# Kernel optimization log

Measured on AMD Instinct MI355X. Metric: run time of the kernel, lower is better.

The kernel has to match this reference:

```python
import jax, jax.numpy as jnp
import numpy as np

B, A, IN, H, NA = 256, 32, 512, 512, 64


def setup_inputs() -> dict:
    key = jax.random.key(0)
    ks = jax.random.split(key, 9)
    s = 1.0 / np.sqrt(H).astype(np.float32)
    si = 1.0 / np.sqrt(IN).astype(np.float32)
    return {
        "inputs": jax.random.normal(ks[0], (B * A, IN), jnp.float32),
        "hidden_state": jnp.zeros((B, A, H), jnp.float32),
        "W1": jax.random.normal(ks[1], (A, H, IN), jnp.float32) * si,
        "b1": jax.random.normal(ks[2], (A, H), jnp.float32) * si,
        "W_ih": jax.random.normal(ks[3], (A, 3 * H, H), jnp.float32) * s,
        "b_ih": jax.random.normal(ks[4], (A, 3 * H), jnp.float32) * s,
        "W_hh": jax.random.normal(ks[5], (A, 3 * H, H), jnp.float32) * s,
        "b_hh": jax.random.normal(ks[6], (A, 3 * H), jnp.float32) * s,
        "W2": jax.random.normal(ks[7], (A, NA, H), jnp.float32) * s,
        "b2": jax.random.normal(ks[8], (A, NA), jnp.float32) * s,
    }


def reference(inputs, hidden_state, W1, b1, W_ih, b_ih, W_hh, b_hh, W2, b2):
    # inputs: [B*A, IN] -> [B, A, IN]; per-agent distinct weights stacked on axis 0 (a)
    x = inputs.reshape(-1, A, IN)
    h_in = hidden_state  # [B, A, H]
    # fc1 + relu, grouped over agents
    x1 = jax.nn.relu(jnp.einsum('bai,ahi->bah', x, W1) + b1)
    # GRUCell (PyTorch gate layout: r, z, n)
    gx = jnp.einsum('bah,agh->bag', x1, W_ih) + b_ih   # [B, A, 3H]
    gh = jnp.einsum('bah,agh->bag', h_in, W_hh) + b_hh  # [B, A, 3H]
    gx_r, gx_z, gx_n = jnp.split(gx, 3, axis=-1)
    gh_r, gh_z, gh_n = jnp.split(gh, 3, axis=-1)
    r = jax.nn.sigmoid(gx_r + gh_r)
    z = jax.nn.sigmoid(gx_z + gh_z)
    n = jnp.tanh(gx_n + r * gh_n)
    h = (1.0 - z) * n + z * h_in  # [B, A, H]
    # fc2 per agent
    q = jnp.einsum('bah,anh->ban', h, W2) + b2  # [B, A, NA]
    # torch: cat(qs, dim=-1).view(-1, n_actions) == reshape to [B*A, NA]
    return q.reshape(-1, NA), h
```

## Files before the change

### kernel.cpp

```cpp
#include <hip/hip_runtime.h>
#include <hip/hip_bf16.h>


typedef __attribute__((ext_vector_type(8))) __bf16 bf16x8;
typedef __attribute__((ext_vector_type(4))) float  f32x4;

constexpr int NAGENT = 32;
constexpr int KC     = 512;

__device__ __forceinline__ bf16x8 cvt8(const float* p) {
  f32x4 u = *(const f32x4*)p;
  f32x4 v = *(const f32x4*)(p + 4);
  bf16x8 w;
  w[0] = (__bf16)u[0]; w[1] = (__bf16)u[1]; w[2] = (__bf16)u[2]; w[3] = (__bf16)u[3];
  w[4] = (__bf16)v[0]; w[5] = (__bf16)v[1]; w[6] = (__bf16)v[2]; w[7] = (__bf16)v[3];
  return w;
}
__device__ __forceinline__ float sigmoid_f(float x) { return 1.f / (1.f + __expf(-x)); }
__device__ __forceinline__ float tanh_f(float x) {
  float xc = fminf(fmaxf(x, -15.f), 15.f);
  float a = __expf(2.f * xc);
  return (a - 1.f) / (a + 1.f);
}
__device__ __forceinline__ int xcd_swz(int bid, int nwg) {
  return (bid & 7) * (nwg >> 3) + (bid >> 3);
}

__global__ __launch_bounds__(512, 4) void gru_k(
    const __bf16* __restrict__ x1, const float* __restrict__ hidden,
    const float* __restrict__ Wih, const float* __restrict__ bih,
    const float* __restrict__ Whh, const float* __restrict__ bhh,
    float* __restrict__ hout, __bf16* __restrict__ hbf) {
  const int wg = xcd_swz(blockIdx.x, gridDim.x);
  const int a  = wg >> 4;
  const int n0 = (wg & 15) * 32;

  __shared__ __attribute__((aligned(16))) __bf16 lB[2][96][8][8];

  const int tid = threadIdx.x;
  const int lane = tid & 63;
  const int wm = tid >> 6;
  const int lr = lane & 15, lk = lane >> 4;

  const int br0 = tid >> 3, bks = tid & 7;
  const int br1 = 64 + (tid >> 3);
  auto wrow = [&](int r) {
    return (size_t)a * 1536 + (r >> 5) * 512 + n0 + (r & 31);
  };
  const size_t boff0 = wrow(br0) * KC + bks * 8;
  const size_t boff1 = (tid < 256 ? wrow(br1) * KC + bks * 8 : 0);

  size_t aBase[2];
#pragma unroll
  for (int i = 0; i < 2; ++i)
    aBase[i] = ((size_t)(wm * 32 + i * 16 + lr) * NAGENT + a) * KC;

  bf16x8 sB0, sB1;
  auto loadB = [&](int t) {
    const float* W = (t < 8) ? Wih : Whh;
    const int kb = (t & 7) * 64;
    sB0 = cvt8(W + boff0 + kb);
    if (tid < 256) sB1 = cvt8(W + boff1 + kb);
  };
  auto writeB = [&](int buf) {
    *(bf16x8*)(&lB[buf][br0][bks ^ (br0 & 7)][0]) = sB0;
    if (tid < 256) *(bf16x8*)(&lB[buf][br1][bks ^ (br1 & 7)][0]) = sB1;
  };

  f32x4 accR[2][2] = {}, accZ[2][2] = {}, accXN[2][2] = {}, accHN[2][2] = {};
  auto computeT = [&](int buf, int t, f32x4 (&accN)[2][2]) {
    const bool ph0 = (t < 8);
    const int kb = (t & 7) * 64;
#pragma unroll
    for (int s = 0; s < 2; ++s) {
      const int ks = s * 4 + lk;
      bf16x8 af[2];
#pragma unroll
      for (int i = 0; i < 2; ++i) {
        const size_t off = aBase[i] + kb + ks * 8;
        af[i] = ph0 ? *(const bf16x8*)(x1 + off) : cvt8(hidden + off);
      }
#pragma unroll
      for (int cc = 0; cc < 2; ++cc) {
        const int rR = 0  + cc * 16 + lr;
        const int rZ = 32 + cc * 16 + lr;
        const int rN = 64 + cc * 16 + lr;
        bf16x8 bR = *(const bf16x8*)(&lB[buf][rR][ks ^ (rR & 7)][0]);
        bf16x8 bZ = *(const bf16x8*)(&lB[buf][rZ][ks ^ (rZ & 7)][0]);
        bf16x8 bN = *(const bf16x8*)(&lB[buf][rN][ks ^ (rN & 7)][0]);
#pragma unroll
        for (int i = 0; i < 2; ++i) {
          accR[i][cc] = __builtin_amdgcn_mfma_f32_16x16x32_bf16(af[i], bR, accR[i][cc], 0, 0, 0);
          accZ[i][cc] = __builtin_amdgcn_mfma_f32_16x16x32_bf16(af[i], bZ, accZ[i][cc], 0, 0, 0);
          accN[i][cc] = __builtin_amdgcn_mfma_f32_16x16x32_bf16(af[i], bN, accN[i][cc], 0, 0, 0);
        }
      }
    }
  };

  loadB(0); writeB(0);
  int cur = 0;
#pragma unroll 1
  for (int t = 0; t < 8; ++t) {
    __syncthreads();
    loadB(t + 1);
    computeT(cur, t, accXN);
    writeB(cur ^ 1); cur ^= 1;
  }
#pragma unroll 1
  for (int t = 8; t < 16; ++t) {
    __syncthreads();
    if (t < 15) loadB(t + 1);
    computeT(cur, t, accHN);
    if (t < 15) { writeB(cur ^ 1); cur ^= 1; }
  }

#pragma unroll
  for (int cc = 0; cc < 2; ++cc) {
    const int col = n0 + cc * 16 + lr;
    const size_t ab = (size_t)a * 1536 + col;
    const float br_ = bih[ab] + bhh[ab];
    const float bz_ = bih[ab + 512] + bhh[ab + 512];
    const float bxn = bih[ab + 1024];
    const float bhn = bhh[ab + 1024];
#pragma unroll
    for (int i = 0; i < 2; ++i) {
      const int r0 = wm * 32 + i * 16 + lk * 4;
#pragma unroll
      for (int e = 0; e < 4; ++e) {
        const size_t o = ((size_t)(r0 + e) * NAGENT + a) * KC + col;
        const float hprev = hidden[o];
        const float r = sigmoid_f(accR[i][cc][e] + br_);
        const float z = sigmoid_f(accZ[i][cc][e] + bz_);
        const float n = tanh_f((accXN[i][cc][e] + bxn) + r * (accHN[i][cc][e] + bhn));
        const float h = (1.f - z) * n + z * hprev;
        hout[o] = h;
        hbf[o] = (__bf16)h;
      }
    }
  }
}

__global__ __launch_bounds__(512, 4) void fc1_k(
    const float* __restrict__ inputs, const float* __restrict__ W1,
    const float* __restrict__ b1, __bf16* __restrict__ x1) {
  const int wg = xcd_swz(blockIdx.x, gridDim.x);
  const int a  = wg >> 3;
  const int n0 = (wg & 7) * 64;

  __shared__ __attribute__((aligned(16))) __bf16 lB[2][64][8][8];

  const int tid = threadIdx.x;
  const int lane = tid & 63;
  const int wm = tid >> 6;
  const int lr = lane & 15, lk = lane >> 4;

  const int brow = tid >> 3, bks = tid & 7;
  const size_t boff = ((size_t)a * 512 + n0 + brow) * KC + bks * 8;

  size_t aBase[2];
#pragma unroll
  for (int i = 0; i < 2; ++i)
    aBase[i] = ((size_t)(wm * 32 + i * 16 + lr) * NAGENT + a) * KC;

  bf16x8 sB;
  auto loadB  = [&](int t) { sB = cvt8(W1 + boff + t * 64); };
  auto writeB = [&](int buf) { *(bf16x8*)(&lB[buf][brow][bks ^ (brow & 7)][0]) = sB; };

  f32x4 acc[2][4] = {};
  auto computeT = [&](int buf, int t) {
    const int kb = t * 64;
#pragma unroll
    for (int s = 0; s < 2; ++s) {
      const int ks = s * 4 + lk;
      bf16x8 af[2];
#pragma unroll
      for (int i = 0; i < 2; ++i)
        af[i] = cvt8(inputs + aBase[i] + kb + ks * 8);
#pragma unroll
      for (int cc = 0; cc < 4; ++cc) {
        const int r = cc * 16 + lr;
        bf16x8 bv = *(const bf16x8*)(&lB[buf][r][ks ^ (r & 7)][0]);
#pragma unroll
        for (int i = 0; i < 2; ++i)
          acc[i][cc] = __builtin_amdgcn_mfma_f32_16x16x32_bf16(af[i], bv, acc[i][cc], 0, 0, 0);
      }
    }
  };

  loadB(0); writeB(0);
  int cur = 0;
#pragma unroll 1
  for (int t = 0; t < 8; ++t) {
    __syncthreads();
    if (t < 7) loadB(t + 1);
    computeT(cur, t);
    if (t < 7) { writeB(cur ^ 1); cur ^= 1; }
  }

#pragma unroll
  for (int cc = 0; cc < 4; ++cc) {
    const int col = n0 + cc * 16 + lr;
    const float bias = b1[(size_t)a * 512 + col];
#pragma unroll
    for (int i = 0; i < 2; ++i) {
      const int r0 = wm * 32 + i * 16 + lk * 4;
#pragma unroll
      for (int e = 0; e < 4; ++e) {
        const float v = fmaxf(acc[i][cc][e] + bias, 0.f);
        x1[((size_t)(r0 + e) * NAGENT + a) * KC + col] = (__bf16)v;
      }
    }
  }
}

template <bool ABF16, int ACT, bool OBF16>
__global__ __launch_bounds__(256) void gemm64(
    const void* __restrict__ Ap, const float* __restrict__ Wp,
    const float* __restrict__ bp, void* __restrict__ Op, const int N) {
  constexpr int BM = 64, MT = 4;
  const int NT = N >> 6;
  const int wg = xcd_swz(blockIdx.x, gridDim.x);
  const int a  = wg / (MT * NT);
  const int rem = wg % (MT * NT);
  const int n0 = (rem / MT) * 64;
  const int b0 = (rem % MT) * BM;

  __shared__ __attribute__((aligned(16))) __bf16 lA[2][4][64][8];
  __shared__ __attribute__((aligned(16))) __bf16 lB[2][4][64][8];

  const int tid = threadIdx.x;
  const int lane = tid & 63;
  const int wn = tid >> 6;
  const int lr = lane & 15, lk = lane >> 4;

  const int ar = tid >> 2, aks = tid & 3;
  const size_t aoff = ((size_t)(b0 + ar) * NAGENT + a) * KC + aks * 8;
  const size_t boff = ((size_t)a * N + n0 + ar) * KC + aks * 8;

  const float*  Af = (const float*)Ap;
  const __bf16* Ab = (const __bf16*)Ap;

  bf16x8 sA, sB;
  auto loadT = [&](int t) {
    if constexpr (ABF16) sA = *(const bf16x8*)(Ab + aoff + t * 32);
    else                 sA = cvt8(Af + aoff + t * 32);
    sB = cvt8(Wp + boff + t * 32);
  };
  auto writeT = [&](int buf) {
    *(bf16x8*)(&lA[buf][aks][ar][0]) = sA;
    *(bf16x8*)(&lB[buf][aks][ar][0]) = sB;
  };

  f32x4 acc[4] = {};
  auto computeT = [&](int buf) {
    bf16x8 bv = *(const bf16x8*)(&lB[buf][lk][wn * 16 + lr][0]);
#pragma unroll
    for (int i = 0; i < 4; ++i) {
      bf16x8 af = *(const bf16x8*)(&lA[buf][lk][i * 16 + lr][0]);
      acc[i] = __builtin_amdgcn_mfma_f32_16x16x32_bf16(af, bv, acc[i], 0, 0, 0);
    }
  };

  loadT(0); writeT(0);
  int cur = 0;
#pragma unroll 1
  for (int t = 0; t < KC / 32; ++t) {
    __syncthreads();
    if (t + 1 < KC / 32) loadT(t + 1);
    computeT(cur);
    if (t + 1 < KC / 32) { writeT(cur ^ 1); cur ^= 1; }
  }

  const int col = n0 + wn * 16 + lr;
  const float bias = bp[(size_t)a * N + col];
#pragma unroll
  for (int i = 0; i < 4; ++i) {
    const int r0 = b0 + i * 16 + lk * 4;
#pragma unroll
    for (int e = 0; e < 4; ++e) {
      float v = acc[i][e] + bias;
      if (ACT == 1) v = fmaxf(v, 0.f);
      const size_t o = ((size_t)(r0 + e) * NAGENT + a) * N + col;
      if constexpr (OBF16) ((__bf16*)Op)[o] = (__bf16)v;
      else                 ((float*)Op)[o]  = v;
    }
  }
}

extern "C" void kernel_launch(void* const* d_in, const int* in_sizes, int n_in,
                              void* d_out, int out_size, void* d_ws, size_t ws_size,
                              hipStream_t stream) {
  const float* inputs = (const float*)d_in[0];
  const float* hidden = (const float*)d_in[1];
  const float* W1   = (const float*)d_in[2];
  const float* b1   = (const float*)d_in[3];
  const float* W_ih = (const float*)d_in[4];
  const float* b_ih = (const float*)d_in[5];
  const float* W_hh = (const float*)d_in[6];
  const float* b_hh = (const float*)d_in[7];
  const float* W2   = (const float*)d_in[8];
  const float* b2   = (const float*)d_in[9];

  float* out_q = (float*)d_out;
  float* out_h = out_q + (size_t)8192 * 64;

  char* ws = (char*)d_ws;
  __bf16* x1  = (__bf16*)(ws);
  __bf16* hbf = (__bf16*)(ws + ((size_t)8 << 20));

  fc1_k<<<256, 512, 0, stream>>>(inputs, W1, b1, x1);
  gru_k<<<512, 512, 0, stream>>>(x1, hidden, W_ih, b_ih, W_hh, b_hh, out_h, hbf);
  gemm64<true, 0, false><<<128, 256, 0, stream>>>(hbf, W2, b2, out_q, 64);
}
```

Baseline: 123.5 us.

## Pack GRU A-operands into MFMA-friendly bf16 layout and stage fc1 inputs in LDS

Adds a prep kernel that converts the hidden state to bf16 in a per-agent, k-chunk-major layout. fc1 now writes its output in the same layout and stages its input tile through LDS using a 2x4 wave tiling. The GRU kernel reads A fragments as contiguous bf16x8 vectors from this packed buffer, software-prefetches them one step ahead in registers, fully unrolls its loops, and takes hprev from the packed bf16 buffer. The aim is to remove scattered fp32 loads and conversions of the hidden state inside the GRU inner loop. The costs are an extra kernel launch, more registers, and hprev being rounded to bf16 in the GRU blend.

```diff
diff --git a/kernel.cpp b/kernel.cpp
--- a/kernel.cpp
+++ b/kernel.cpp
@@ -26,8 +26,108 @@
   return (bid & 7) * (nwg >> 3) + (bid >> 3);
 }
 
+
+__global__ __launch_bounds__(256) void prep_k(
+    const float* __restrict__ hidden, __bf16* __restrict__ AF) {
+  const int idx = blockIdx.x * 256 + threadIdx.x;
+  const int kc = idx & 63;
+  const int row = idx >> 6;
+  const int a = row & 31, b = row >> 5;
+  bf16x8 v = cvt8(hidden + (size_t)row * KC + kc * 8);
+  *(bf16x8*)(AF + ((size_t)(a * 128 + 64 + kc) * 256 + b) * 8) = v;
+}
+
+__global__ __launch_bounds__(512, 2) void fc1_k(
+    const float* __restrict__ inputs, const float* __restrict__ W1,
+    const float* __restrict__ b1, __bf16* __restrict__ AF) {
+  const int wg = xcd_swz(blockIdx.x, gridDim.x);
+  const int a  = wg >> 3;
+  const int n0 = (wg & 7) * 64;
+
+  __shared__ __attribute__((aligned(16))) __bf16 lA[2][256][8][8];
+  __shared__ __attribute__((aligned(16))) __bf16 lB[2][64][8][8];
+
+  const int tid = threadIdx.x;
+  const int lane = tid & 63;
+  const int wave = tid >> 6;
+  const int wm = wave >> 1, wn = wave & 1;
+  const int lr = lane & 15, lk = lane >> 4;
+
+  int arow[4], aks[4]; size_t aoff[4];
+#pragma unroll
+  for (int c = 0; c < 4; ++c) {
+    const int idx = c * 512 + tid;
+    arow[c] = idx >> 3; aks[c] = idx & 7;
+    aoff[c] = ((size_t)arow[c] * NAGENT + a) * KC + aks[c] * 8;
+  }
+  const int brow = tid >> 3, bks = tid & 7;
+  const size_t boff = ((size_t)a * 512 + n0 + brow) * KC + bks * 8;
+
+  bf16x8 sA[4], sB;
+  auto loadT = [&](int t) {
+    const int kb = t * 64;
+#pragma unroll
+    for (int c = 0; c < 4; ++c) sA[c] = cvt8(inputs + aoff[c] + kb);
+    sB = cvt8(W1 + boff + kb);
+  };
+  auto writeT = [&](int buf) {
+#pragma unroll
+    for (int c = 0; c < 4; ++c)
+      *(bf16x8*)(&lA[buf][arow[c]][aks[c] ^ (arow[c] & 7)][0]) = sA[c];
+    *(bf16x8*)(&lB[buf][brow][bks ^ (brow & 7)][0]) = sB;
+  };
+
+  f32x4 acc[4][2] = {};
+  auto computeT = [&](int buf) {
+#pragma unroll
+    for (int s = 0; s < 2; ++s) {
+      const int ks = s * 4 + lk;
+      bf16x8 af[4];
+#pragma unroll
+      for (int i = 0; i < 4; ++i) {
+        const int row = wm * 64 + i * 16 + lr;
+        af[i] = *(const bf16x8*)(&lA[buf][row][ks ^ (row & 7)][0]);
+      }
+#pragma unroll
+      for (int cb = 0; cb < 2; ++cb) {
+        const int br = wn * 32 + cb * 16 + lr;
+        bf16x8 bv = *(const bf16x8*)(&lB[buf][br][ks ^ (br & 7)][0]);
+#pragma unroll
+        for (int i = 0; i < 4; ++i)
+          acc[i][cb] = __builtin_amdgcn_mfma_f32_16x16x32_bf16(af[i], bv, acc[i][cb], 0, 0, 0);
+      }
+    }
+  };
+
+  loadT(0); writeT(0);
+  int cur = 0;
+#pragma unroll 1
+  for (int t = 0; t < 8; ++t) {
+    __syncthreads();
+    if (t < 7) loadT(t + 1);
+    computeT(cur);
+    if (t < 7) { writeT(cur ^ 1); cur ^= 1; }
+  }
+
+#pragma unroll
+  for (int cb = 0; cb < 2; ++cb) {
+    const int col = n0 + wn * 32 + cb * 16 + lr;
+    const int kc = col >> 3, c7 = col & 7;
+    const float bias = b1[(size_t)a * 512 + col];
+#pragma unroll
+    for (int i = 0; i < 4; ++i) {
+      const int r0 = wm * 64 + i * 16 + lk * 4;
+#pragma unroll
+      for (int e = 0; e < 4; ++e) {
+        const float v = fmaxf(acc[i][cb][e] + bias, 0.f);
+        AF[((size_t)(a * 128 + kc) * 256 + r0 + e) * 8 + c7] = (__bf16)v;
+      }
+    }
+  }
+}
+
 __global__ __launch_bounds__(512, 4) void gru_k(
-    const __bf16* __restrict__ x1, const float* __restrict__ hidden,
+    const __bf16* __restrict__ AF,
     const float* __restrict__ Wih, const float* __restrict__ bih,
     const float* __restrict__ Whh, const float* __restrict__ bhh,
     float* __restrict__ hout, __bf16* __restrict__ hbf) {
@@ -53,7 +153,8 @@
   size_t aBase[2];
 #pragma unroll
   for (int i = 0; i < 2; ++i)
-    aBase[i] = ((size_t)(wm * 32 + i * 16 + lr) * NAGENT + a) * KC;
+    aBase[i] = (size_t)a * 262144 + (size_t)lk * 2048 +
+               (size_t)(wm * 32 + i * 16 + lr) * 8;
 
   bf16x8 sB0, sB1;
   auto loadB = [&](int t) {
@@ -67,52 +168,54 @@
     if (tid < 256) *(bf16x8*)(&lB[buf][br1][bks ^ (br1 & 7)][0]) = sB1;
   };
 
+  bf16x8 af0[2][2], af1[2][2];
+  auto loadA = [&](bf16x8 (&dst)[2][2], int t) {
+#pragma unroll
+    for (int s = 0; s < 2; ++s)
+#pragma unroll
+      for (int i = 0; i < 2; ++i)
+        dst[s][i] = *(const bf16x8*)(AF + aBase[i] + (size_t)t * 16384 + s * 8192);
+  };
+
   f32x4 accR[2][2] = {}, accZ[2][2] = {}, accXN[2][2] = {}, accHN[2][2] = {};
-  auto computeT = [&](int buf, int t, f32x4 (&accN)[2][2]) {
-    const bool ph0 = (t < 8);
-    const int kb = (t & 7) * 64;
+  auto compute = [&](int buf, bf16x8 (&af)[2][2], f32x4 (&accN)[2][2]) {
 #pragma unroll
     for (int s = 0; s < 2; ++s) {
       const int ks = s * 4 + lk;
-      bf16x8 af[2];
-#pragma unroll
-      for (int i = 0; i < 2; ++i) {
-        const size_t off = aBase[i] + kb + ks * 8;
-        af[i] = ph0 ? *(const bf16x8*)(x1 + off) : cvt8(hidden + off);
-      }
 #pragma unroll
       for (int cc = 0; cc < 2; ++cc) {
-        const int rR = 0  + cc * 16 + lr;
-        const int rZ = 32 + cc * 16 + lr;
-        const int rN = 64 + cc * 16 + lr;
-        bf16x8 bR = *(const bf16x8*)(&lB[buf][rR][ks ^ (rR & 7)][0]);
-        bf16x8 bZ = *(const bf16x8*)(&lB[buf][rZ][ks ^ (rZ & 7)][0]);
-        bf16x8 bN = *(const bf16x8*)(&lB[buf][rN][ks ^ (rN & 7)][0]);
+        const int rr = cc * 16 + lr;
+        const int sw = ks ^ (rr & 7);
+        bf16x8 bR = *(const bf16x8*)(&lB[buf][rr][sw][0]);
+        bf16x8 bZ = *(const bf16x8*)(&lB[buf][32 + rr][sw][0]);
+        bf16x8 bN = *(const bf16x8*)(&lB[buf][64 + rr][sw][0]);
 #pragma unroll
         for (int i = 0; i < 2; ++i) {
-          accR[i][cc] = __builtin_amdgcn_mfma_f32_16x16x32_bf16(af[i], bR, accR[i][cc], 0, 0, 0);
-          accZ[i][cc] = __builtin_amdgcn_mfma_f32_16x16x32_bf16(af[i], bZ, accZ[i][cc], 0, 0, 0);
-          accN[i][cc] = __builtin_amdgcn_mfma_f32_16x16x32_bf16(af[i], bN, accN[i][cc], 0, 0, 0);
+          accR[i][cc] = __builtin_amdgcn_mfma_f32_16x16x32_bf16(af[s][i], bR, accR[i][cc], 0, 0, 0);
+          accZ[i][cc] = __builtin_amdgcn_mfma_f32_16x16x32_bf16(af[s][i], bZ, accZ[i][cc], 0, 0, 0);
+          accN[i][cc] = __builtin_amdgcn_mfma_f32_16x16x32_bf16(af[s][i], bN, accN[i][cc], 0, 0, 0);
         }
       }
     }
   };
 
   loadB(0); writeB(0);
-  int cur = 0;
-#pragma unroll 1
+  loadA(af0, 0);
+#pragma unroll
   for (int t = 0; t < 8; ++t) {
     __syncthreads();
     loadB(t + 1);
-    computeT(cur, t, accXN);
-    writeB(cur ^ 1); cur ^= 1;
-  }
-#pragma unroll 1
+    if (t & 1) { loadA(af0, t + 1); compute(1, af1, accXN); }
+    else       { loadA(af1, t + 1); compute(0, af0, accXN); }
+    writeB((t & 1) ^ 1);
+  }
+#pragma unroll
   for (int t = 8; t < 16; ++t) {
     __syncthreads();
     if (t < 15) loadB(t + 1);
-    computeT(cur, t, accHN);
-    if (t < 15) { writeB(cur ^ 1); cur ^= 1; }
+    if (t & 1) { if (t < 15) loadA(af0, t + 1); compute(1, af1, accHN); }
+    else       { if (t < 15) loadA(af1, t + 1); compute(0, af0, accHN); }
+    if (t < 15) writeB((t & 1) ^ 1);
   }
 
 #pragma unroll
@@ -123,92 +226,20 @@
     const float bz_ = bih[ab + 512] + bhh[ab + 512];
     const float bxn = bih[ab + 1024];
     const float bhn = bhh[ab + 1024];
+    const size_t hfb = ((size_t)(a * 128 + 64 + (col >> 3)) * 256) * 8 + (col & 7);
 #pragma unroll
     for (int i = 0; i < 2; ++i) {
       const int r0 = wm * 32 + i * 16 + lk * 4;
 #pragma unroll
       for (int e = 0; e < 4; ++e) {
-        const size_t o = ((size_t)(r0 + e) * NAGENT + a) * KC + col;
-        const float hprev = hidden[o];
+        const float hprev = (float)AF[hfb + (size_t)(r0 + e) * 8];
         const float r = sigmoid_f(accR[i][cc][e] + br_);
         const float z = sigmoid_f(accZ[i][cc][e] + bz_);
         const float n = tanh_f((accXN[i][cc][e] + bxn) + r * (accHN[i][cc][e] + bhn));
         const float h = (1.f - z) * n + z * hprev;
+        const size_t o = ((size_t)(r0 + e) * NAGENT + a) * KC + col;
         hout[o] = h;
         hbf[o] = (__bf16)h;
-      }
-    }
-  }
-}
-
-__global__ __launch_bounds__(512, 4) void fc1_k(
-    const float* __restrict__ inputs, const float* __restrict__ W1,
-    const float* __restrict__ b1, __bf16* __restrict__ x1) {
-  const int wg = xcd_swz(blockIdx.x, gridDim.x);
-  const int a  = wg >> 3;
-  const int n0 = (wg & 7) * 64;
-
-  __shared__ __attribute__((aligned(16))) __bf16 lB[2][64][8][8];
-
-  const int tid = threadIdx.x;
-  const int lane = tid & 63;
-  const int wm = tid >> 6;
-  const int lr = lane & 15, lk = lane >> 4;
-
-  const int brow = tid >> 3, bks = tid & 7;
-  const size_t boff = ((size_t)a * 512 + n0 + brow) * KC + bks * 8;
-
-  size_t aBase[2];
-#pragma unroll
-  for (int i = 0; i < 2; ++i)
-    aBase[i] = ((size_t)(wm * 32 + i * 16 + lr) * NAGENT + a) * KC;
-
-  bf16x8 sB;
-  auto loadB  = [&](int t) { sB = cvt8(W1 + boff + t * 64); };
-  auto writeB = [&](int buf) { *(bf16x8*)(&lB[buf][brow][bks ^ (brow & 7)][0]) = sB; };
-
-  f32x4 acc[2][4] = {};
-  auto computeT = [&](int buf, int t) {
-    const int kb = t * 64;
-#pragma unroll
-    for (int s = 0; s < 2; ++s) {
-      const int ks = s * 4 + lk;
-      bf16x8 af[2];
-#pragma unroll
-      for (int i = 0; i < 2; ++i)
-        af[i] = cvt8(inputs + aBase[i] + kb + ks * 8);
-#pragma unroll
-      for (int cc = 0; cc < 4; ++cc) {
-        const int r = cc * 16 + lr;
-        bf16x8 bv = *(const bf16x8*)(&lB[buf][r][ks ^ (r & 7)][0]);
-#pragma unroll
-        for (int i = 0; i < 2; ++i)
-          acc[i][cc] = __builtin_amdgcn_mfma_f32_16x16x32_bf16(af[i], bv, acc[i][cc], 0, 0, 0);
-      }
-    }
-  };
-
-  loadB(0); writeB(0);
-  int cur = 0;
-#pragma unroll 1
-  for (int t = 0; t < 8; ++t) {
-    __syncthreads();
-    if (t < 7) loadB(t + 1);
-    computeT(cur, t);
-    if (t < 7) { writeB(cur ^ 1); cur ^= 1; }
-  }
-
-#pragma unroll
-  for (int cc = 0; cc < 4; ++cc) {
-    const int col = n0 + cc * 16 + lr;
-    const float bias = b1[(size_t)a * 512 + col];
-#pragma unroll
-    for (int i = 0; i < 2; ++i) {
-      const int r0 = wm * 32 + i * 16 + lk * 4;
-#pragma unroll
-      for (int e = 0; e < 4; ++e) {
-        const float v = fmaxf(acc[i][cc][e] + bias, 0.f);
-        x1[((size_t)(r0 + e) * NAGENT + a) * KC + col] = (__bf16)v;
       }
     }
   }
@@ -306,10 +337,11 @@
   float* out_h = out_q + (size_t)8192 * 64;
 
   char* ws = (char*)d_ws;
-  __bf16* x1  = (__bf16*)(ws);
-  __bf16* hbf = (__bf16*)(ws + ((size_t)8 << 20));
-
-  fc1_k<<<256, 512, 0, stream>>>(inputs, W1, b1, x1);
-  gru_k<<<512, 512, 0, stream>>>(x1, hidden, W_ih, b_ih, W_hh, b_hh, out_h, hbf);
+  __bf16* AF  = (__bf16*)(ws);
+  __bf16* hbf = (__bf16*)(ws + ((size_t)16 << 20));
+
+  prep_k<<<2048, 256, 0, stream>>>(hidden, AF);
+  fc1_k<<<256, 512, 0, stream>>>(inputs, W1, b1, AF);
+  gru_k<<<512, 512, 0, stream>>>(AF, W_ih, b_ih, W_hh, b_hh, out_h, hbf);
   gemm64<true, 0, false><<<128, 256, 0, stream>>>(hbf, W2, b2, out_q, 64);
 }
```

Result: faster. 115.0 us (-6.8%).
